# Performance work log

Hardware: AMD Instinct MI355X
Metric: run time of the kernel (lower is better)

The kernel has to match this reference:

```python
import jax, jax.numpy as jnp
import numpy as np

N_NODES = 10000
N_EDGES = 320000
D_IN = 256
D_OUT = 256


def setup_inputs() -> dict:
    key = jax.random.key(0)
    k1, k2, k3, k4, k5, k6 = jax.random.split(key, 6)
    feat = jax.random.normal(k1, (N_NODES, D_IN), dtype=jnp.float32)
    eweight = jax.random.uniform(k2, (N_EDGES, 1), dtype=jnp.float32)
    # Linear(in_dim*2 -> out_dim): weight [out, 2*in], bias [out]
    W = jax.random.normal(k3, (D_OUT, 2 * D_IN), dtype=jnp.float32) / np.sqrt(2 * D_IN)
    b = jax.random.normal(k4, (D_OUT,), dtype=jnp.float32) * 0.01
    src = jax.random.randint(k5, (N_EDGES,), 0, N_NODES, dtype=jnp.int64)
    dst = jax.random.randint(k6, (N_EDGES,), 0, N_NODES, dtype=jnp.int64)
    return {"feat": feat, "eweight": eweight, "W": W, "b": b, "src": src, "dst": dst}


def reference(feat, eweight, W, b, src, dst):
    n = feat.shape[0]
    # message: u_mul_e -> h[src] * ew   (broadcast [E,1] over [E,D])
    msg = feat[src] * eweight
    # mean reduce by destination: sum(msg) / in-degree
    agg = jax.ops.segment_sum(msg, dst, num_segments=n)
    deg = jax.ops.segment_sum(jnp.ones((src.shape[0],), dtype=feat.dtype), dst, num_segments=n)
    h_neigh = agg / jnp.maximum(deg, 1.0)[:, None]
    # concat aggregated with self features, then linear
    h = jnp.concatenate([h_neigh, feat], axis=-1)  # [N, 2*D]
    return h @ W.T + b
```

## Files before the change

### kernel.cpp

```cpp
#include <hip/hip_runtime.h>
#include <hip/hip_bf16.h>

#define N_NODES 10000
#define N_EDGES 320000
#define D 256
#define K_TOT 512
#define CAP 128

typedef __attribute__((ext_vector_type(8))) short bf16x8;
typedef __attribute__((ext_vector_type(4))) float f32x4;

__device__ __forceinline__ float bf2f(unsigned short u) {
  return __uint_as_float(((unsigned int)u) << 16);
}
__device__ __forceinline__ unsigned short f2bf(float f) {
  unsigned int x = __float_as_uint(f);
  unsigned int r = (x + 0x7fffu + ((x >> 16) & 1u)) >> 16;
  return (unsigned short)r;
}

#define FEAT_VECS (N_NODES * D / 8)
#define W_VECS    (D * K_TOT / 8)
#define CUR_VECS  (N_NODES / 4)
__global__ __launch_bounds__(256) void tobf16_kernel(
    const float* __restrict__ feat, const float* __restrict__ W,
    unsigned short* __restrict__ hcat, unsigned short* __restrict__ Wb,
    int* __restrict__ cursor) {
  int gid = blockIdx.x * 256 + threadIdx.x;
  const float* srcp;
  unsigned short* dstp;
  if (gid < FEAT_VECS) {
    int row = gid >> 5;
    int v = gid & 31;
    srcp = feat + (size_t)row * D + v * 8;
    dstp = hcat + (size_t)row * K_TOT + D + v * 8;
  } else if (gid < FEAT_VECS + W_VECS) {
    int g = gid - FEAT_VECS;
    int row = g >> 6;
    int v = g & 63;
    srcp = W + (size_t)row * K_TOT + v * 8;
    dstp = Wb + (size_t)row * K_TOT + v * 8;
  } else if (gid < FEAT_VECS + W_VECS + CUR_VECS) {
    int g = gid - (FEAT_VECS + W_VECS);
    reinterpret_cast<int4*>(cursor)[g] = make_int4(0, 0, 0, 0);
    return;
  } else {
    return;
  }
  float4 a = reinterpret_cast<const float4*>(srcp)[0];
  float4 b = reinterpret_cast<const float4*>(srcp)[1];
  reinterpret_cast<ushort4*>(dstp)[0] =
      make_ushort4(f2bf(a.x), f2bf(a.y), f2bf(a.z), f2bf(a.w));
  reinterpret_cast<ushort4*>(dstp)[1] =
      make_ushort4(f2bf(b.x), f2bf(b.y), f2bf(b.z), f2bf(b.w));
}

__global__ __launch_bounds__(256) void append_kernel(const int* __restrict__ src,
                                                     const int* __restrict__ dst,
                                                     const float* __restrict__ ew,
                                                     int* __restrict__ cursor,
                                                     int2* __restrict__ bucket) {
  int i = (blockIdx.x * 256 + threadIdx.x) * 2;
  if (i + 1 < N_EDGES) {
    int2 s2 = *reinterpret_cast<const int2*>(src + i);
    int2 d2 = *reinterpret_cast<const int2*>(dst + i);
    float2 w2 = *reinterpret_cast<const float2*>(ew + i);
    int pos0 = atomicAdd(&cursor[d2.x], 1);
    if (pos0 < CAP)
      bucket[(size_t)d2.x * CAP + pos0] = make_int2(s2.x, __float_as_int(w2.x));
    int pos1 = atomicAdd(&cursor[d2.y], 1);
    if (pos1 < CAP)
      bucket[(size_t)d2.y * CAP + pos1] = make_int2(s2.y, __float_as_int(w2.y));
  } else if (i < N_EDGES) {
    int d = dst[i];
    int pos = atomicAdd(&cursor[d], 1);
    if (pos < CAP)
      bucket[(size_t)d * CAP + pos] = make_int2(src[i], __float_as_int(ew[i]));
  }
}

__global__ __launch_bounds__(256) void agg_kernel(const int* __restrict__ cursor,
                                                  const int2* __restrict__ bucket,
                                                  unsigned short* __restrict__ hcat) {
  int node = (blockIdx.x * 256 + threadIdx.x) >> 6;
  int lane = threadIdx.x & 63;
  if (node >= N_NODES) return;
  int cnt = cursor[node];
  int end = min(cnt, CAP);
  const int2* bk = bucket + (size_t)node * CAP;
  const unsigned short* fb = hcat + D + (size_t)lane * 4;
  float acc0 = 0.f, acc1 = 0.f, acc2 = 0.f, acc3 = 0.f;
  int i = 0;

#define GATHER2(p, va, vb)                                                     \
    va = *reinterpret_cast<const ushort4*>(fb + (size_t)(p).x * K_TOT);        \
    vb = *reinterpret_cast<const ushort4*>(fb + (size_t)(p).z * K_TOT);
#define ACC1(v, wgt)                                                           \
    acc0 += bf2f((v).x) * (wgt); acc1 += bf2f((v).y) * (wgt);                  \
    acc2 += bf2f((v).z) * (wgt); acc3 += bf2f((v).w) * (wgt);
#define ACCP(p, va, vb)                                                        \
    { float wa_ = __int_as_float((p).y), wb_ = __int_as_float((p).w);          \
      ACC1(va, wa_) ACC1(vb, wb_) }

  for (; i + 16 <= end; i += 16) {
    int4 p0 = *reinterpret_cast<const int4*>(bk + i);
    int4 p1 = *reinterpret_cast<const int4*>(bk + i + 2);
    int4 p2 = *reinterpret_cast<const int4*>(bk + i + 4);
    int4 p3 = *reinterpret_cast<const int4*>(bk + i + 6);
    int4 p4 = *reinterpret_cast<const int4*>(bk + i + 8);
    int4 p5 = *reinterpret_cast<const int4*>(bk + i + 10);
    int4 p6 = *reinterpret_cast<const int4*>(bk + i + 12);
    int4 p7 = *reinterpret_cast<const int4*>(bk + i + 14);
    ushort4 v0, v1, v2, v3, v4, v5, v6, v7, v8, v9, va, vb, vc, vd, ve, vf;
    GATHER2(p0, v0, v1) GATHER2(p1, v2, v3) GATHER2(p2, v4, v5) GATHER2(p3, v6, v7)
    GATHER2(p4, v8, v9) GATHER2(p5, va, vb) GATHER2(p6, vc, vd) GATHER2(p7, ve, vf)
    ACCP(p0, v0, v1) ACCP(p1, v2, v3) ACCP(p2, v4, v5) ACCP(p3, v6, v7)
    ACCP(p4, v8, v9) ACCP(p5, va, vb) ACCP(p6, vc, vd) ACCP(p7, ve, vf)
  }
  for (; i + 8 <= end; i += 8) {
    int4 p0 = *reinterpret_cast<const int4*>(bk + i);
    int4 p1 = *reinterpret_cast<const int4*>(bk + i + 2);
    int4 p2 = *reinterpret_cast<const int4*>(bk + i + 4);
    int4 p3 = *reinterpret_cast<const int4*>(bk + i + 6);
    ushort4 v0, v1, v2, v3, v4, v5, v6, v7;
    GATHER2(p0, v0, v1) GATHER2(p1, v2, v3) GATHER2(p2, v4, v5) GATHER2(p3, v6, v7)
    ACCP(p0, v0, v1) ACCP(p1, v2, v3) ACCP(p2, v4, v5) ACCP(p3, v6, v7)
  }
  for (; i < end; ++i) {
    int2 sw = bk[i];
    ushort4 v = *reinterpret_cast<const ushort4*>(fb + (size_t)sw.x * K_TOT);
    float wgt = __int_as_float(sw.y);
    ACC1(v, wgt)
  }
#undef GATHER2
#undef ACC1
#undef ACCP

  float inv = 1.0f / fmaxf((float)cnt, 1.0f);
  ushort4 o = make_ushort4(f2bf(acc0 * inv), f2bf(acc1 * inv),
                           f2bf(acc2 * inv), f2bf(acc3 * inv));
  *reinterpret_cast<ushort4*>(hcat + (size_t)node * K_TOT + lane * 4) = o;
}

#define GBM 64
#define GBN 64
#define GBK 64
#define LPAD 72
#define RTILES 157

__global__ __launch_bounds__(256) void gemm_kernel(
    const unsigned short* __restrict__ hcat, const unsigned short* __restrict__ Wb,
    const float* __restrict__ bias, float* __restrict__ out) {
  __shared__ unsigned short As[GBM][LPAD];
  __shared__ unsigned short Bs[GBN][LPAD];

  int bid = blockIdx.x;
  int r, c;
  if (bid < 608) {
    int g = bid >> 5;
    int w8 = bid & 31;
    r = g * 8 + (w8 & 7);
    c = w8 >> 3;
  } else {
    int w8 = bid - 608;
    r = 152 + w8 % 5;
    c = w8 / 5;
  }
  int row0 = r * GBM;
  int col0 = c * GBN;

  int t = threadIdx.x;
  int lane = t & 63;
  int w = t >> 6;
  int wr = w >> 1;
  int wc = w & 1;
  int lhi = lane >> 4;
  int llo = lane & 15;

  f32x4 acc[2][2];
  #pragma unroll
  for (int m = 0; m < 2; ++m)
    #pragma unroll
    for (int n = 0; n < 2; ++n) acc[m][n] = (f32x4){0.f, 0.f, 0.f, 0.f};

  for (int k0 = 0; k0 < K_TOT; k0 += GBK) {
    #pragma unroll
    for (int it = 0; it < 2; ++it) {
      int idx = t + it * 256;
      int rr = idx >> 3;
      int kv = (idx & 7) * 8;
      int row = row0 + rr;
      uint4 v = make_uint4(0, 0, 0, 0);
      if (row < N_NODES)
        v = *reinterpret_cast<const uint4*>(hcat + (size_t)row * K_TOT + k0 + kv);
      *reinterpret_cast<uint4*>(&As[rr][kv]) = v;
    }
    #pragma unroll
    for (int it = 0; it < 2; ++it) {
      int idx = t + it * 256;
      int cc = idx >> 3;
      int kv = (idx & 7) * 8;
      uint4 v = *reinterpret_cast<const uint4*>(Wb + (size_t)(col0 + cc) * K_TOT + k0 + kv);
      *reinterpret_cast<uint4*>(&Bs[cc][kv]) = v;
    }
    __syncthreads();

    #pragma unroll
    for (int ks = 0; ks < 2; ++ks) {
      int ak = ks * 32 + lhi * 8;
      bf16x8 a[2], b[2];
      #pragma unroll
      for (int m = 0; m < 2; ++m)
        a[m] = *reinterpret_cast<const bf16x8*>(&As[wr * 32 + m * 16 + llo][ak]);
      #pragma unroll
      for (int n = 0; n < 2; ++n)
        b[n] = *reinterpret_cast<const bf16x8*>(&Bs[wc * 32 + n * 16 + llo][ak]);
      #pragma unroll
      for (int m = 0; m < 2; ++m)
        #pragma unroll
        for (int n = 0; n < 2; ++n)
          acc[m][n] = __builtin_amdgcn_mfma_f32_16x16x32_bf16(a[m], b[n], acc[m][n], 0, 0, 0);
    }
    __syncthreads();
  }

  #pragma unroll
  for (int m = 0; m < 2; ++m) {
    #pragma unroll
    for (int n = 0; n < 2; ++n) {
      int col = col0 + wc * 32 + n * 16 + llo;
      float bv = bias[col];
      #pragma unroll
      for (int rr = 0; rr < 4; ++rr) {
        int orow = row0 + wr * 32 + m * 16 + lhi * 4 + rr;
        if (orow < N_NODES)
          out[(size_t)orow * D + col] = acc[m][n][rr] + bv;
      }
    }
  }
}

extern "C" void kernel_launch(void* const* d_in, const int* in_sizes, int n_in,
                              void* d_out, int out_size, void* d_ws, size_t ws_size,
                              hipStream_t stream) {
  const float* feat = (const float*)d_in[0];
  const float* ew   = (const float*)d_in[1];
  const float* W    = (const float*)d_in[2];
  const float* bias = (const float*)d_in[3];
  const int*   src  = (const int*)d_in[4];
  const int*   dst  = (const int*)d_in[5];
  float* out = (float*)d_out;

  char* ws = (char*)d_ws;
  unsigned short* hcat = (unsigned short*)ws;  ws += (size_t)N_NODES * K_TOT * sizeof(unsigned short);
  unsigned short* Wb   = (unsigned short*)ws;  ws += (size_t)D * K_TOT * sizeof(unsigned short);
  int* cursor   = (int*)ws;                    ws += N_NODES * sizeof(int);
  int2* bucket  = (int2*)ws;                   ws += (size_t)N_NODES * CAP * sizeof(int2);

  tobf16_kernel<<<(FEAT_VECS + W_VECS + CUR_VECS + 255) / 256, 256, 0, stream>>>(
      feat, W, hcat, Wb, cursor);
  append_kernel<<<(N_EDGES / 2 + 255) / 256, 256, 0, stream>>>(src, dst, ew, cursor, bucket);
  agg_kernel<<<(N_NODES * 64 + 255) / 256, 256, 0, stream>>>(cursor, bucket, hcat);

  gemm_kernel<<<RTILES * 4, 256, 0, stream>>>(hcat, Wb, bias, out);
}
```

Baseline: 71.63 us.

## Fuse aggregation and GEMM into one kernel with per-row-tile completion flags

Merges the aggregation and GEMM kernels into a single launch. The first 2500 blocks aggregate neighbours and bump a per-64-row done counter with release semantics. The GEMM blocks first compute the self-feature half of K, then spin on their row tile's counter before computing the aggregated half. This removes one launch and kernel boundary and overlaps the GEMM with aggregation. The spin-wait is only deadlock-free because the aggregation blocks have lower block indices and are scheduled first. The 16-step unrolled aggregation loop is also dropped, leaving the 8-step one.

```diff
diff --git a/kernel.cpp b/kernel.cpp
--- a/kernel.cpp
+++ b/kernel.cpp
@@ -21,11 +21,11 @@
 
 #define FEAT_VECS (N_NODES * D / 8)
 #define W_VECS    (D * K_TOT / 8)
-#define CUR_VECS  (N_NODES / 4)
+#define ZERO_VECS ((N_NODES + 160) / 4)
 __global__ __launch_bounds__(256) void tobf16_kernel(
     const float* __restrict__ feat, const float* __restrict__ W,
     unsigned short* __restrict__ hcat, unsigned short* __restrict__ Wb,
-    int* __restrict__ cursor) {
+    int* __restrict__ cursor ) {
   int gid = blockIdx.x * 256 + threadIdx.x;
   const float* srcp;
   unsigned short* dstp;
@@ -40,7 +40,7 @@
     int v = g & 63;
     srcp = W + (size_t)row * K_TOT + v * 8;
     dstp = Wb + (size_t)row * K_TOT + v * 8;
-  } else if (gid < FEAT_VECS + W_VECS + CUR_VECS) {
+  } else if (gid < FEAT_VECS + W_VECS + ZERO_VECS) {
     int g = gid - (FEAT_VECS + W_VECS);
     reinterpret_cast<int4*>(cursor)[g] = make_int4(0, 0, 0, 0);
     return;
@@ -79,18 +79,30 @@
   }
 }
 
-__global__ __launch_bounds__(256) void agg_kernel(const int* __restrict__ cursor,
-                                                  const int2* __restrict__ bucket,
-                                                  unsigned short* __restrict__ hcat) {
-  int node = (blockIdx.x * 256 + threadIdx.x) >> 6;
-  int lane = threadIdx.x & 63;
-  if (node >= N_NODES) return;
-  int cnt = cursor[node];
-  int end = min(cnt, CAP);
-  const int2* bk = bucket + (size_t)node * CAP;
-  const unsigned short* fb = hcat + D + (size_t)lane * 4;
-  float acc0 = 0.f, acc1 = 0.f, acc2 = 0.f, acc3 = 0.f;
-  int i = 0;
+#define AGG_BLKS 2500
+#define GBM 64
+#define GBN 64
+#define GBK 64
+#define LPAD 72
+#define RTILES 157
+
+__global__ __launch_bounds__(256) void aggemm_kernel(
+    const int* __restrict__ cursor, const int2* __restrict__ bucket,
+    unsigned short* __restrict__ hcat, const unsigned short* __restrict__ Wb,
+    const float* __restrict__ bias, float* __restrict__ out,
+    int* __restrict__ done) {
+  __shared__ unsigned short As[GBM][LPAD];
+  __shared__ unsigned short Bs[GBN][LPAD];
+
+  if (blockIdx.x < AGG_BLKS) {
+    int node = (blockIdx.x << 2) + (threadIdx.x >> 6);
+    int lane = threadIdx.x & 63;
+    int cnt = cursor[node];
+    int end = min(cnt, CAP);
+    const int2* bk = bucket + (size_t)node * CAP;
+    const unsigned short* fb = hcat + D + (size_t)lane * 4;
+    float acc0 = 0.f, acc1 = 0.f, acc2 = 0.f, acc3 = 0.f;
+    int i = 0;
 
 #define GATHER2(p, va, vb)                                                     \
     va = *reinterpret_cast<const ushort4*>(fb + (size_t)(p).x * K_TOT);        \
@@ -102,59 +114,39 @@
     { float wa_ = __int_as_float((p).y), wb_ = __int_as_float((p).w);          \
       ACC1(va, wa_) ACC1(vb, wb_) }
 
-  for (; i + 16 <= end; i += 16) {
-    int4 p0 = *reinterpret_cast<const int4*>(bk + i);
-    int4 p1 = *reinterpret_cast<const int4*>(bk + i + 2);
-    int4 p2 = *reinterpret_cast<const int4*>(bk + i + 4);
-    int4 p3 = *reinterpret_cast<const int4*>(bk + i + 6);
-    int4 p4 = *reinterpret_cast<const int4*>(bk + i + 8);
-    int4 p5 = *reinterpret_cast<const int4*>(bk + i + 10);
-    int4 p6 = *reinterpret_cast<const int4*>(bk + i + 12);
-    int4 p7 = *reinterpret_cast<const int4*>(bk + i + 14);
-    ushort4 v0, v1, v2, v3, v4, v5, v6, v7, v8, v9, va, vb, vc, vd, ve, vf;
-    GATHER2(p0, v0, v1) GATHER2(p1, v2, v3) GATHER2(p2, v4, v5) GATHER2(p3, v6, v7)
-    GATHER2(p4, v8, v9) GATHER2(p5, va, vb) GATHER2(p6, vc, vd) GATHER2(p7, ve, vf)
-    ACCP(p0, v0, v1) ACCP(p1, v2, v3) ACCP(p2, v4, v5) ACCP(p3, v6, v7)
-    ACCP(p4, v8, v9) ACCP(p5, va, vb) ACCP(p6, vc, vd) ACCP(p7, ve, vf)
-  }
-  for (; i + 8 <= end; i += 8) {
-    int4 p0 = *reinterpret_cast<const int4*>(bk + i);
-    int4 p1 = *reinterpret_cast<const int4*>(bk + i + 2);
-    int4 p2 = *reinterpret_cast<const int4*>(bk + i + 4);
-    int4 p3 = *reinterpret_cast<const int4*>(bk + i + 6);
-    ushort4 v0, v1, v2, v3, v4, v5, v6, v7;
-    GATHER2(p0, v0, v1) GATHER2(p1, v2, v3) GATHER2(p2, v4, v5) GATHER2(p3, v6, v7)
-    ACCP(p0, v0, v1) ACCP(p1, v2, v3) ACCP(p2, v4, v5) ACCP(p3, v6, v7)
-  }
-  for (; i < end; ++i) {
-    int2 sw = bk[i];
-    ushort4 v = *reinterpret_cast<const ushort4*>(fb + (size_t)sw.x * K_TOT);
-    float wgt = __int_as_float(sw.y);
-    ACC1(v, wgt)
-  }
+    for (; i + 8 <= end; i += 8) {
+      int4 p0 = *reinterpret_cast<const int4*>(bk + i);
+      int4 p1 = *reinterpret_cast<const int4*>(bk + i + 2);
+      int4 p2 = *reinterpret_cast<const int4*>(bk + i + 4);
+      int4 p3 = *reinterpret_cast<const int4*>(bk + i + 6);
+      ushort4 v0, v1, v2, v3, v4, v5, v6, v7;
+      GATHER2(p0, v0, v1) GATHER2(p1, v2, v3) GATHER2(p2, v4, v5) GATHER2(p3, v6, v7)
+      ACCP(p0, v0, v1) ACCP(p1, v2, v3) ACCP(p2, v4, v5) ACCP(p3, v6, v7)
+    }
+    for (; i < end; ++i) {
+      int2 sw = bk[i];
+      ushort4 v = *reinterpret_cast<const ushort4*>(fb + (size_t)sw.x * K_TOT);
+      float wgt = __int_as_float(sw.y);
+      ACC1(v, wgt)
+    }
 #undef GATHER2
 #undef ACC1
 #undef ACCP
 
-  float inv = 1.0f / fmaxf((float)cnt, 1.0f);
-  ushort4 o = make_ushort4(f2bf(acc0 * inv), f2bf(acc1 * inv),
-                           f2bf(acc2 * inv), f2bf(acc3 * inv));
-  *reinterpret_cast<ushort4*>(hcat + (size_t)node * K_TOT + lane * 4) = o;
-}
-
-#define GBM 64
-#define GBN 64
-#define GBK 64
-#define LPAD 72
-#define RTILES 157
-
-__global__ __launch_bounds__(256) void gemm_kernel(
-    const unsigned short* __restrict__ hcat, const unsigned short* __restrict__ Wb,
-    const float* __restrict__ bias, float* __restrict__ out) {
-  __shared__ unsigned short As[GBM][LPAD];
-  __shared__ unsigned short Bs[GBN][LPAD];
-
-  int bid = blockIdx.x;
+    float inv = 1.0f / fmaxf((float)cnt, 1.0f);
+    ushort4 o = make_ushort4(f2bf(acc0 * inv), f2bf(acc1 * inv),
+                             f2bf(acc2 * inv), f2bf(acc3 * inv));
+    *reinterpret_cast<ushort4*>(hcat + (size_t)node * K_TOT + lane * 4) = o;
+
+    __syncthreads();
+    if (threadIdx.x == 0) {
+      __hip_atomic_fetch_add(&done[blockIdx.x >> 4], 1,
+                             __ATOMIC_RELEASE, __HIP_MEMORY_SCOPE_AGENT);
+    }
+    return;
+  }
+
+  int bid = blockIdx.x - AGG_BLKS;
   int r, c;
   if (bid < 608) {
     int g = bid >> 5;
@@ -183,46 +175,60 @@
     #pragma unroll
     for (int n = 0; n < 2; ++n) acc[m][n] = (f32x4){0.f, 0.f, 0.f, 0.f};
 
-  for (int k0 = 0; k0 < K_TOT; k0 += GBK) {
-    #pragma unroll
-    for (int it = 0; it < 2; ++it) {
-      int idx = t + it * 256;
-      int rr = idx >> 3;
-      int kv = (idx & 7) * 8;
-      int row = row0 + rr;
-      uint4 v = make_uint4(0, 0, 0, 0);
-      if (row < N_NODES)
-        v = *reinterpret_cast<const uint4*>(hcat + (size_t)row * K_TOT + k0 + kv);
-      *reinterpret_cast<uint4*>(&As[rr][kv]) = v;
-    }
-    #pragma unroll
-    for (int it = 0; it < 2; ++it) {
-      int idx = t + it * 256;
-      int cc = idx >> 3;
-      int kv = (idx & 7) * 8;
-      uint4 v = *reinterpret_cast<const uint4*>(Wb + (size_t)(col0 + cc) * K_TOT + k0 + kv);
-      *reinterpret_cast<uint4*>(&Bs[cc][kv]) = v;
-    }
-    __syncthreads();
-
-    #pragma unroll
-    for (int ks = 0; ks < 2; ++ks) {
-      int ak = ks * 32 + lhi * 8;
-      bf16x8 a[2], b[2];
-      #pragma unroll
-      for (int m = 0; m < 2; ++m)
-        a[m] = *reinterpret_cast<const bf16x8*>(&As[wr * 32 + m * 16 + llo][ak]);
-      #pragma unroll
-      for (int n = 0; n < 2; ++n)
-        b[n] = *reinterpret_cast<const bf16x8*>(&Bs[wc * 32 + n * 16 + llo][ak]);
-      #pragma unroll
-      for (int m = 0; m < 2; ++m)
-        #pragma unroll
-        for (int n = 0; n < 2; ++n)
-          acc[m][n] = __builtin_amdgcn_mfma_f32_16x16x32_bf16(a[m], b[n], acc[m][n], 0, 0, 0);
-    }
-    __syncthreads();
-  }
+#define GEMM_KSTEP(k0)                                                         \
+  {                                                                            \
+    _Pragma("unroll")                                                          \
+    for (int it = 0; it < 2; ++it) {                                           \
+      int idx = t + it * 256;                                                  \
+      int rr = idx >> 3;                                                       \
+      int kv = (idx & 7) * 8;                                                  \
+      int row = row0 + rr;                                                     \
+      uint4 v = make_uint4(0, 0, 0, 0);                                        \
+      if (row < N_NODES)                                                       \
+        v = *reinterpret_cast<const uint4*>(hcat + (size_t)row * K_TOT + (k0) + kv); \
+      *reinterpret_cast<uint4*>(&As[rr][kv]) = v;                              \
+    }                                                                          \
+    _Pragma("unroll")                                                          \
+    for (int it = 0; it < 2; ++it) {                                           \
+      int idx = t + it * 256;                                                  \
+      int cc = idx >> 3;                                                       \
+      int kv = (idx & 7) * 8;                                                  \
+      uint4 v = *reinterpret_cast<const uint4*>(                               \
+          Wb + (size_t)(col0 + cc) * K_TOT + (k0) + kv);                       \
+      *reinterpret_cast<uint4*>(&Bs[cc][kv]) = v;                              \
+    }                                                                          \
+    __syncthreads();                                                           \
+    _Pragma("unroll")                                                          \
+    for (int ks = 0; ks < 2; ++ks) {                                           \
+      int ak = ks * 32 + lhi * 8;                                              \
+      bf16x8 a[2], b[2];                                                       \
+      _Pragma("unroll")                                                        \
+      for (int m = 0; m < 2; ++m)                                              \
+        a[m] = *reinterpret_cast<const bf16x8*>(&As[wr * 32 + m * 16 + llo][ak]); \
+      _Pragma("unroll")                                                        \
+      for (int n = 0; n < 2; ++n)                                              \
+        b[n] = *reinterpret_cast<const bf16x8*>(&Bs[wc * 32 + n * 16 + llo][ak]); \
+      _Pragma("unroll")                                                        \
+      for (int m = 0; m < 2; ++m)                                              \
+        _Pragma("unroll")                                                      \
+        for (int n = 0; n < 2; ++n)                                            \
+          acc[m][n] = __builtin_amdgcn_mfma_f32_16x16x32_bf16(a[m], b[n], acc[m][n], 0, 0, 0); \
+    }                                                                          \
+    __syncthreads();                                                           \
+  }
+
+  for (int k0 = D; k0 < K_TOT; k0 += GBK) GEMM_KSTEP(k0)
+
+  if (t == 0) {
+    int target = min(16, AGG_BLKS - (r << 4));
+    while (__hip_atomic_load(&done[r], __ATOMIC_ACQUIRE,
+                             __HIP_MEMORY_SCOPE_AGENT) < target)
+      __builtin_amdgcn_s_sleep(8);
+  }
+  __syncthreads();
+
+  for (int k0 = 0; k0 < D; k0 += GBK) GEMM_KSTEP(k0)
+#undef GEMM_KSTEP
 
   #pragma unroll
   for (int m = 0; m < 2; ++m) {
@@ -255,12 +261,12 @@
   unsigned short* hcat = (unsigned short*)ws;  ws += (size_t)N_NODES * K_TOT * sizeof(unsigned short);
   unsigned short* Wb   = (unsigned short*)ws;  ws += (size_t)D * K_TOT * sizeof(unsigned short);
   int* cursor   = (int*)ws;                    ws += N_NODES * sizeof(int);
+  int* done     = (int*)ws;                    ws += 160 * sizeof(int);
   int2* bucket  = (int2*)ws;                   ws += (size_t)N_NODES * CAP * sizeof(int2);
 
-  tobf16_kernel<<<(FEAT_VECS + W_VECS + CUR_VECS + 255) / 256, 256, 0, stream>>>(
+  tobf16_kernel<<<(FEAT_VECS + W_VECS + ZERO_VECS + 255) / 256, 256, 0, stream>>>(
       feat, W, hcat, Wb, cursor);
   append_kernel<<<(N_EDGES / 2 + 255) / 256, 256, 0, stream>>>(src, dst, ew, cursor, bucket);
-  agg_kernel<<<(N_NODES * 64 + 255) / 256, 256, 0, stream>>>(cursor, bucket, hcat);
-
-  gemm_kernel<<<RTILES * 4, 256, 0, stream>>>(hcat, Wb, bias, out);
-}
+  aggemm_kernel<<<AGG_BLKS + RTILES * 4, 256, 0, stream>>>(
+      cursor, bucket, hcat, Wb, bias, out, done);
+}
```

New measurement: 120.0 us. 67.5% more time.

## Fuse neighbor aggregation and linear GEMM into one kernel per 16-node tile

Applied to the files above, without the earlier changes.

Merges the aggregation and GEMM kernels: each block aggregates 16 nodes into a shared-memory row tile holding both the neighbor mean and the self features, then multiplies it by the full weight matrix with MFMA, reading W straight from global memory. This removes the hcat round trip through global memory and one kernel launch, and shrinks the bf16 feature buffer to a compact layout. In exchange, each block reloads the entire 256x512 weight matrix from global or L2 with no shared-memory staging, and the aggregation loop loses its 16-wide unroll.

```diff
diff --git a/kernel.cpp b/kernel.cpp
--- a/kernel.cpp
+++ b/kernel.cpp
@@ -24,22 +24,18 @@
 #define CUR_VECS  (N_NODES / 4)
 __global__ __launch_bounds__(256) void tobf16_kernel(
     const float* __restrict__ feat, const float* __restrict__ W,
-    unsigned short* __restrict__ hcat, unsigned short* __restrict__ Wb,
+    unsigned short* __restrict__ featb, unsigned short* __restrict__ Wb,
     int* __restrict__ cursor) {
   int gid = blockIdx.x * 256 + threadIdx.x;
   const float* srcp;
   unsigned short* dstp;
   if (gid < FEAT_VECS) {
-    int row = gid >> 5;
-    int v = gid & 31;
-    srcp = feat + (size_t)row * D + v * 8;
-    dstp = hcat + (size_t)row * K_TOT + D + v * 8;
+    srcp = feat + (size_t)gid * 8;
+    dstp = featb + (size_t)gid * 8;
   } else if (gid < FEAT_VECS + W_VECS) {
     int g = gid - FEAT_VECS;
-    int row = g >> 6;
-    int v = g & 63;
-    srcp = W + (size_t)row * K_TOT + v * 8;
-    dstp = Wb + (size_t)row * K_TOT + v * 8;
+    srcp = W + (size_t)g * 8;
+    dstp = Wb + (size_t)g * 8;
   } else if (gid < FEAT_VECS + W_VECS + CUR_VECS) {
     int g = gid - (FEAT_VECS + W_VECS);
     reinterpret_cast<int4*>(cursor)[g] = make_int4(0, 0, 0, 0);
@@ -79,22 +75,32 @@
   }
 }
 
-__global__ __launch_bounds__(256) void agg_kernel(const int* __restrict__ cursor,
-                                                  const int2* __restrict__ bucket,
-                                                  unsigned short* __restrict__ hcat) {
-  int node = (blockIdx.x * 256 + threadIdx.x) >> 6;
-  int lane = threadIdx.x & 63;
-  if (node >= N_NODES) return;
-  int cnt = cursor[node];
-  int end = min(cnt, CAP);
-  const int2* bk = bucket + (size_t)node * CAP;
-  const unsigned short* fb = hcat + D + (size_t)lane * 4;
-  float acc0 = 0.f, acc1 = 0.f, acc2 = 0.f, acc3 = 0.f;
-  int i = 0;
+#define LPAD2 520
+
+__global__ __launch_bounds__(256) void aggemm_kernel(
+    const int* __restrict__ cursor, const int2* __restrict__ bucket,
+    const unsigned short* __restrict__ featb, const unsigned short* __restrict__ Wb,
+    const float* __restrict__ bias, float* __restrict__ out) {
+  __shared__ unsigned short Ah[16][LPAD2];
+
+  int t = threadIdx.x;
+  int w = t >> 6;
+  int lane = t & 63;
+  int node0 = blockIdx.x * 16;
+
+  const unsigned short* fb = featb + (size_t)lane * 4;
+  for (int j = 0; j < 4; ++j) {
+    int local = (w << 2) + j;
+    int node = node0 + local;
+    int cnt = cursor[node];
+    int end = min(cnt, CAP);
+    const int2* bk = bucket + (size_t)node * CAP;
+    float acc0 = 0.f, acc1 = 0.f, acc2 = 0.f, acc3 = 0.f;
+    int i = 0;
 
 #define GATHER2(p, va, vb)                                                     \
-    va = *reinterpret_cast<const ushort4*>(fb + (size_t)(p).x * K_TOT);        \
-    vb = *reinterpret_cast<const ushort4*>(fb + (size_t)(p).z * K_TOT);
+    va = *reinterpret_cast<const ushort4*>(fb + (size_t)(p).x * D);            \
+    vb = *reinterpret_cast<const ushort4*>(fb + (size_t)(p).z * D);
 #define ACC1(v, wgt)                                                           \
     acc0 += bf2f((v).x) * (wgt); acc1 += bf2f((v).y) * (wgt);                  \
     acc2 += bf2f((v).z) * (wgt); acc3 += bf2f((v).w) * (wgt);
@@ -102,140 +108,65 @@
     { float wa_ = __int_as_float((p).y), wb_ = __int_as_float((p).w);          \
       ACC1(va, wa_) ACC1(vb, wb_) }
 
-  for (; i + 16 <= end; i += 16) {
-    int4 p0 = *reinterpret_cast<const int4*>(bk + i);
-    int4 p1 = *reinterpret_cast<const int4*>(bk + i + 2);
-    int4 p2 = *reinterpret_cast<const int4*>(bk + i + 4);
-    int4 p3 = *reinterpret_cast<const int4*>(bk + i + 6);
-    int4 p4 = *reinterpret_cast<const int4*>(bk + i + 8);
-    int4 p5 = *reinterpret_cast<const int4*>(bk + i + 10);
-    int4 p6 = *reinterpret_cast<const int4*>(bk + i + 12);
-    int4 p7 = *reinterpret_cast<const int4*>(bk + i + 14);
-    ushort4 v0, v1, v2, v3, v4, v5, v6, v7, v8, v9, va, vb, vc, vd, ve, vf;
-    GATHER2(p0, v0, v1) GATHER2(p1, v2, v3) GATHER2(p2, v4, v5) GATHER2(p3, v6, v7)
-    GATHER2(p4, v8, v9) GATHER2(p5, va, vb) GATHER2(p6, vc, vd) GATHER2(p7, ve, vf)
-    ACCP(p0, v0, v1) ACCP(p1, v2, v3) ACCP(p2, v4, v5) ACCP(p3, v6, v7)
-    ACCP(p4, v8, v9) ACCP(p5, va, vb) ACCP(p6, vc, vd) ACCP(p7, ve, vf)
-  }
-  for (; i + 8 <= end; i += 8) {
-    int4 p0 = *reinterpret_cast<const int4*>(bk + i);
-    int4 p1 = *reinterpret_cast<const int4*>(bk + i + 2);
-    int4 p2 = *reinterpret_cast<const int4*>(bk + i + 4);
-    int4 p3 = *reinterpret_cast<const int4*>(bk + i + 6);
-    ushort4 v0, v1, v2, v3, v4, v5, v6, v7;
-    GATHER2(p0, v0, v1) GATHER2(p1, v2, v3) GATHER2(p2, v4, v5) GATHER2(p3, v6, v7)
-    ACCP(p0, v0, v1) ACCP(p1, v2, v3) ACCP(p2, v4, v5) ACCP(p3, v6, v7)
-  }
-  for (; i < end; ++i) {
-    int2 sw = bk[i];
-    ushort4 v = *reinterpret_cast<const ushort4*>(fb + (size_t)sw.x * K_TOT);
-    float wgt = __int_as_float(sw.y);
-    ACC1(v, wgt)
-  }
+    for (; i + 8 <= end; i += 8) {
+      int4 p0 = *reinterpret_cast<const int4*>(bk + i);
+      int4 p1 = *reinterpret_cast<const int4*>(bk + i + 2);
+      int4 p2 = *reinterpret_cast<const int4*>(bk + i + 4);
+      int4 p3 = *reinterpret_cast<const int4*>(bk + i + 6);
+      ushort4 v0, v1, v2, v3, v4, v5, v6, v7;
+      GATHER2(p0, v0, v1) GATHER2(p1, v2, v3) GATHER2(p2, v4, v5) GATHER2(p3, v6, v7)
+      ACCP(p0, v0, v1) ACCP(p1, v2, v3) ACCP(p2, v4, v5) ACCP(p3, v6, v7)
+    }
+    for (; i < end; ++i) {
+      int2 sw = bk[i];
+      ushort4 v = *reinterpret_cast<const ushort4*>(fb + (size_t)sw.x * D);
+      float wgt = __int_as_float(sw.y);
+      ACC1(v, wgt)
+    }
 #undef GATHER2
 #undef ACC1
 #undef ACCP
 
-  float inv = 1.0f / fmaxf((float)cnt, 1.0f);
-  ushort4 o = make_ushort4(f2bf(acc0 * inv), f2bf(acc1 * inv),
-                           f2bf(acc2 * inv), f2bf(acc3 * inv));
-  *reinterpret_cast<ushort4*>(hcat + (size_t)node * K_TOT + lane * 4) = o;
-}
-
-#define GBM 64
-#define GBN 64
-#define GBK 64
-#define LPAD 72
-#define RTILES 157
-
-__global__ __launch_bounds__(256) void gemm_kernel(
-    const unsigned short* __restrict__ hcat, const unsigned short* __restrict__ Wb,
-    const float* __restrict__ bias, float* __restrict__ out) {
-  __shared__ unsigned short As[GBM][LPAD];
-  __shared__ unsigned short Bs[GBN][LPAD];
-
-  int bid = blockIdx.x;
-  int r, c;
-  if (bid < 608) {
-    int g = bid >> 5;
-    int w8 = bid & 31;
-    r = g * 8 + (w8 & 7);
-    c = w8 >> 3;
-  } else {
-    int w8 = bid - 608;
-    r = 152 + w8 % 5;
-    c = w8 / 5;
-  }
-  int row0 = r * GBM;
-  int col0 = c * GBN;
-
-  int t = threadIdx.x;
-  int lane = t & 63;
-  int w = t >> 6;
-  int wr = w >> 1;
-  int wc = w & 1;
-  int lhi = lane >> 4;
-  int llo = lane & 15;
-
-  f32x4 acc[2][2];
-  #pragma unroll
-  for (int m = 0; m < 2; ++m)
-    #pragma unroll
-    for (int n = 0; n < 2; ++n) acc[m][n] = (f32x4){0.f, 0.f, 0.f, 0.f};
-
-  for (int k0 = 0; k0 < K_TOT; k0 += GBK) {
-    #pragma unroll
-    for (int it = 0; it < 2; ++it) {
-      int idx = t + it * 256;
-      int rr = idx >> 3;
-      int kv = (idx & 7) * 8;
-      int row = row0 + rr;
-      uint4 v = make_uint4(0, 0, 0, 0);
-      if (row < N_NODES)
-        v = *reinterpret_cast<const uint4*>(hcat + (size_t)row * K_TOT + k0 + kv);
-      *reinterpret_cast<uint4*>(&As[rr][kv]) = v;
-    }
-    #pragma unroll
-    for (int it = 0; it < 2; ++it) {
-      int idx = t + it * 256;
-      int cc = idx >> 3;
-      int kv = (idx & 7) * 8;
-      uint4 v = *reinterpret_cast<const uint4*>(Wb + (size_t)(col0 + cc) * K_TOT + k0 + kv);
-      *reinterpret_cast<uint4*>(&Bs[cc][kv]) = v;
-    }
-    __syncthreads();
-
-    #pragma unroll
-    for (int ks = 0; ks < 2; ++ks) {
-      int ak = ks * 32 + lhi * 8;
-      bf16x8 a[2], b[2];
-      #pragma unroll
-      for (int m = 0; m < 2; ++m)
-        a[m] = *reinterpret_cast<const bf16x8*>(&As[wr * 32 + m * 16 + llo][ak]);
-      #pragma unroll
-      for (int n = 0; n < 2; ++n)
-        b[n] = *reinterpret_cast<const bf16x8*>(&Bs[wc * 32 + n * 16 + llo][ak]);
-      #pragma unroll
-      for (int m = 0; m < 2; ++m)
-        #pragma unroll
-        for (int n = 0; n < 2; ++n)
-          acc[m][n] = __builtin_amdgcn_mfma_f32_16x16x32_bf16(a[m], b[n], acc[m][n], 0, 0, 0);
-    }
-    __syncthreads();
+    float inv = 1.0f / fmaxf((float)cnt, 1.0f);
+    ushort4 o = make_ushort4(f2bf(acc0 * inv), f2bf(acc1 * inv),
+                             f2bf(acc2 * inv), f2bf(acc3 * inv));
+    *reinterpret_cast<ushort4*>(&Ah[local][lane * 4]) = o;
   }
 
   #pragma unroll
-  for (int m = 0; m < 2; ++m) {
+  for (int it = 0; it < 2; ++it) {
+    int idx = t + it * 256;
+    int r = idx >> 5;
+    int v = idx & 31;
+    uint4 x = *reinterpret_cast<const uint4*>(featb + (size_t)(node0 + r) * D + v * 8);
+    *reinterpret_cast<uint4*>(&Ah[r][D + v * 8]) = x;
+  }
+  __syncthreads();
+
+  int lhi = lane >> 4;
+  int llo = lane & 15;
+  f32x4 acc[4];
+  #pragma unroll
+  for (int n = 0; n < 4; ++n) acc[n] = (f32x4){0.f, 0.f, 0.f, 0.f};
+
+  const unsigned short* wb0 = Wb + (size_t)(w * 64 + llo) * K_TOT + lhi * 8;
+  #pragma unroll
+  for (int ks = 0; ks < 16; ++ks) {
+    bf16x8 a = *reinterpret_cast<const bf16x8*>(&Ah[llo][ks * 32 + lhi * 8]);
     #pragma unroll
-    for (int n = 0; n < 2; ++n) {
-      int col = col0 + wc * 32 + n * 16 + llo;
-      float bv = bias[col];
-      #pragma unroll
-      for (int rr = 0; rr < 4; ++rr) {
-        int orow = row0 + wr * 32 + m * 16 + lhi * 4 + rr;
-        if (orow < N_NODES)
-          out[(size_t)orow * D + col] = acc[m][n][rr] + bv;
-      }
+    for (int n = 0; n < 4; ++n) {
+      bf16x8 b = *reinterpret_cast<const bf16x8*>(wb0 + (size_t)(n * 16) * K_TOT + ks * 32);
+      acc[n] = __builtin_amdgcn_mfma_f32_16x16x32_bf16(a, b, acc[n], 0, 0, 0);
+    }
+  }
+
+  #pragma unroll
+  for (int n = 0; n < 4; ++n) {
+    int col = w * 64 + n * 16 + llo;
+    float bv = bias[col];
+    #pragma unroll
+    for (int r = 0; r < 4; ++r) {
+      out[(size_t)(node0 + lhi * 4 + r) * D + col] = acc[n][r] + bv;
     }
   }
 }
@@ -252,15 +183,13 @@
   float* out = (float*)d_out;
 
   char* ws = (char*)d_ws;
-  unsigned short* hcat = (unsigned short*)ws;  ws += (size_t)N_NODES * K_TOT * sizeof(unsigned short);
-  unsigned short* Wb   = (unsigned short*)ws;  ws += (size_t)D * K_TOT * sizeof(unsigned short);
+  unsigned short* featb = (unsigned short*)ws; ws += (size_t)N_NODES * D * sizeof(unsigned short);
+  unsigned short* Wb    = (unsigned short*)ws; ws += (size_t)D * K_TOT * sizeof(unsigned short);
   int* cursor   = (int*)ws;                    ws += N_NODES * sizeof(int);
   int2* bucket  = (int2*)ws;                   ws += (size_t)N_NODES * CAP * sizeof(int2);
 
   tobf16_kernel<<<(FEAT_VECS + W_VECS + CUR_VECS + 255) / 256, 256, 0, stream>>>(
-      feat, W, hcat, Wb, cursor);
+      feat, W, featb, Wb, cursor);
   append_kernel<<<(N_EDGES / 2 + 255) / 256, 256, 0, stream>>>(src, dst, ew, cursor, bucket);
-  agg_kernel<<<(N_NODES * 64 + 255) / 256, 256, 0, stream>>>(cursor, bucket, hcat);
-
-  gemm_kernel<<<RTILES * 4, 256, 0, stream>>>(hcat, Wb, bias, out);
+  aggemm_kernel<<<N_NODES / 16, 256, 0, stream>>>(cursor, bucket, featb, Wb, bias, out);
 }
```

New measurement: 86.08 us. 1.2x slower.
